# Kernel optimization log

Measured on AMD Instinct MI355X. Metric: run time of the kernel, lower is better.

The kernel has to match this reference:

```python
import jax, jax.numpy as jnp
import numpy as np

N = 100000      # nodes
E = 400000      # edges (before self loops)
D_ATOM = 98
D_BOND = 13
EMB = 128
HEADS = 4
L = 4           # num_layer


def prelu(x, a):
    return jnp.where(x >= 0, x, a * x)


def setup_inputs() -> dict:
    key = jax.random.key(0)
    ks = jax.random.split(key, 12)
    s = 0.05
    inp = {
        "x": jax.random.normal(ks[0], (N, D_ATOM), dtype=jnp.float32),
        "edge_index": jax.random.randint(ks[1], (2, E), 0, N, dtype=jnp.int64),
        "edge_attr": jax.random.uniform(ks[2], (E, D_BOND), dtype=jnp.float32),
        # GNN-level params
        "x_emb_W": jax.random.normal(ks[3], (D_ATOM, EMB), dtype=jnp.float32) * s,
        "prelu_gnn": jnp.float32(0.25),
        # per-layer GATConv params, stacked on leading layer axis
        "wl_W": jax.random.normal(ks[4], (L, EMB, HEADS * EMB), dtype=jnp.float32) * s,
        "wl_b": jnp.zeros((L, HEADS * EMB), dtype=jnp.float32),
        "att": jax.random.normal(ks[5], (L, HEADS, 2 * EMB), dtype=jnp.float32) * s,
        "gat_bias": jnp.zeros((L, EMB), dtype=jnp.float32),
        "ee_W": jax.random.normal(ks[6], (L, D_BOND, HEADS * EMB), dtype=jnp.float32) * s,
        "ee_b": jnp.zeros((L, HEADS * EMB), dtype=jnp.float32),
        "prelu_gat": jnp.full((L,), 0.25, dtype=jnp.float32),
        # LayerNorm params per layer
        "ln_g": jnp.ones((L, EMB), dtype=jnp.float32),
        "ln_b": jnp.zeros((L, EMB), dtype=jnp.float32),
    }
    return inp


def reference(x, edge_index, edge_attr, x_emb_W, prelu_gnn, wl_W, wl_b, att,
              gat_bias, ee_W, ee_b, prelu_gat, ln_g, ln_b):
    # add self loops: (i, i) for every node; self-loop edge_attr = zeros
    loop = jnp.arange(N, dtype=edge_index.dtype)
    src = jnp.concatenate([edge_index[0], loop])  # [E+N] source (j)
    dst = jnp.concatenate([edge_index[1], loop])  # [E+N] target (i)
    ea = jnp.concatenate(
        [edge_attr, jnp.zeros((N, D_BOND), dtype=edge_attr.dtype)], axis=0)

    # input embedding + shared PReLU
    h = prelu(x @ x_emb_W, prelu_gnn)  # [N, EMB]

    for l in range(L):
        a = prelu_gat[l]
        ee = prelu(ea @ ee_W[l] + ee_b[l], a)       # [E+N, H*EMB]
        xw = prelu(h @ wl_W[l] + wl_b[l], a)        # [N, H*EMB]
        x_i = xw[dst].reshape(-1, HEADS, EMB)       # target feats
        x_j = (xw[src] + ee).reshape(-1, HEADS, EMB)  # source feats + edge emb
        # attention logits: cat([x_i,x_j]) . att
        alpha = (x_i * att[l, :, :EMB]).sum(-1) + (x_j * att[l, :, EMB:]).sum(-1)
        alpha = prelu(alpha, a)                     # [E+N, HEADS]
        # segment softmax grouped by src (edge_index[0]), as in the module
        m = jax.ops.segment_max(alpha, src, num_segments=N)
        alpha = jnp.exp(alpha - m[src])
        ssum = jax.ops.segment_sum(alpha, src, num_segments=N)
        alpha = alpha / (ssum[src] + 1e-16)
        # weighted messages, scatter-add to target nodes
        msg = (x_j * alpha[:, :, None]).reshape(-1, HEADS * EMB)
        aggr = jax.ops.segment_sum(msg, dst, num_segments=N)
        aggr = aggr.reshape(N, HEADS, EMB).mean(axis=1) + gat_bias[l]
        # LayerNorm
        mu = aggr.mean(-1, keepdims=True)
        var = ((aggr - mu) ** 2).mean(-1, keepdims=True)
        hn = (aggr - mu) / jnp.sqrt(var + 1e-5) * ln_g[l] + ln_b[l]
        # dropout is identity (drop_ratio=0); PReLU on all but last layer
        h = hn if l == L - 1 else prelu(hn, prelu_gnn)

    return h  # JK='last'
```

## Files before the change

### kernel.cpp

```cpp
#include <hip/hip_runtime.h>
#include <stdint.h>

#define NN 100000
#define NE 400000
#define NT 500000
#define DA 98
#define DB 13
#define EMB 128
#define HE 512
#define NWAVE 8192
#define IMSK 0x0FFFFFFF

typedef unsigned short ushort_t;
typedef __bf16 bf16x8 __attribute__((ext_vector_type(8)));
typedef float floatx4 __attribute__((ext_vector_type(4)));
typedef __fp16 fp16v2 __attribute__((ext_vector_type(2)));

__device__ __forceinline__ float prelu_f(float x, float a) { return x >= 0.f ? x : a * x; }

__device__ __forceinline__ ushort_t f2bf(float f) {
    unsigned u = __float_as_uint(f);
    unsigned r = (u + 0x7fffu + ((u >> 16) & 1u)) >> 16;
    return (ushort_t)r;
}
__device__ __forceinline__ float bflo(unsigned u) { return __uint_as_float(u << 16); }
__device__ __forceinline__ float bfhi(unsigned u) { return __uint_as_float(u & 0xffff0000u); }

__device__ __forceinline__ float dot2(unsigned a, unsigned b, float c) {
    return __builtin_amdgcn_fdot2(__builtin_bit_cast(fp16v2, a), __builtin_bit_cast(fp16v2, b), c, false);
}

__device__ __forceinline__ unsigned pk2(float lo, float hi) {
    fp16v2 p = __builtin_amdgcn_cvt_pkrtz(lo, hi);
    return __builtin_bit_cast(unsigned, p);
}

__global__ void k_count(const int* __restrict__ ei, int* __restrict__ sc, int* __restrict__ dc) {
    int e = blockIdx.x * 256 + threadIdx.x;
    if (e >= NT) return;
    int s, d;
    if (e < NE) { s = ei[e]; d = ei[NE + e]; } else { s = d = e - NE; }
    atomicAdd(sc + s, 1);
    atomicAdd(dc + d, 1);
}

__global__ void k_scan1(const int* __restrict__ cnt, int* __restrict__ part, int* __restrict__ bsum) {
    __shared__ int tmp[512];
    int t = threadIdx.x, i = blockIdx.x * 512 + t;
    int v = (i < NN) ? cnt[i] : 0;
    tmp[t] = v;
    __syncthreads();
    for (int off = 1; off < 512; off <<= 1) {
        int x = (t >= off) ? tmp[t - off] : 0;
        __syncthreads();
        tmp[t] += x;
        __syncthreads();
    }
    if (i < NN) part[i] = tmp[t] - v;
    if (t == 511) bsum[blockIdx.x] = tmp[t];
}

__global__ void k_scan2(int* __restrict__ bsum, int nb) {
    __shared__ int tmp[256];
    int t = threadIdx.x;
    int v = (t < nb) ? bsum[t] : 0;
    tmp[t] = v;
    __syncthreads();
    for (int off = 1; off < 256; off <<= 1) {
        int x = (t >= off) ? tmp[t - off] : 0;
        __syncthreads();
        tmp[t] += x;
        __syncthreads();
    }
    if (t < nb) bsum[t] = tmp[t] - v;
}

__global__ void k_scan3(const int* __restrict__ part, const int* __restrict__ bsum,
                        int* __restrict__ off, int* __restrict__ cur) {
    int i = blockIdx.x * 256 + threadIdx.x;
    if (i < NN) {
        int v = part[i] + bsum[i >> 9];
        off[i] = v;
        cur[i] = v;
    }
    if (i == 0) off[NN] = NT;
}

__global__ void k_fill(const int* __restrict__ ei, int* __restrict__ scur, int* __restrict__ dcur,
                       int* __restrict__ seid, int* __restrict__ deid) {
    int e = blockIdx.x * 256 + threadIdx.x;
    if (e >= NT) return;
    int s, d;
    if (e < NE) { s = ei[e]; d = ei[NE + e]; } else { s = d = e - NE; }
    seid[atomicAdd(scur + s, 1)] = e;
    deid[atomicAdd(dcur + d, 1)] = e;
}

__global__ void k_invperm(const int* __restrict__ seid, int* __restrict__ s2p) {
    int i = blockIdx.x * 256 + threadIdx.x;
    if (i < NT) s2p[seid[i]] = i;
}

__global__ void k_wrange(const int* __restrict__ offs, int* __restrict__ nstart) {
    int w = blockIdx.x * 256 + threadIdx.x;
    if (w > NWAVE) return;
    long long target = (long long)w * NT / NWAVE;
    int lo = 0, hi = NN;
    while (lo < hi) {
        int mid = (lo + hi) >> 1;
        if ((long long)offs[mid] < target) lo = mid + 1; else hi = mid;
    }
    nstart[w] = lo;
}

__global__ void k_dprep(const int* __restrict__ deid, const int* __restrict__ ei,
                        const float* __restrict__ ea, const int* __restrict__ s2p,
                        int* __restrict__ src_d, int* __restrict__ d2s,
                        unsigned* __restrict__ ea_d) {
    int i = blockIdx.x * 256 + threadIdx.x;
    if (i >= NT + 4) return;
    unsigned p[8] = {0, 0, 0, 0, 0, 0, 0, 0};
    int s = 0, pos = 0;
    if (i < NT) {
        int eid = deid[i];
        if (eid < NE) {
            s = ei[eid];
            float v[DB];
            #pragma unroll
            for (int k = 0; k < DB; ++k) v[k] = ea[(size_t)eid * DB + k];
            #pragma unroll
            for (int kp = 0; kp < 6; ++kp) p[kp] = pk2(v[2 * kp], v[2 * kp + 1]);
            p[6] = pk2(v[12], 0.f);
        } else {
            s = (eid - NE) | (1 << 30);
        }
        pos = s2p[eid];
    }
    uint4* o = (uint4*)&ea_d[(size_t)i * 8];
    o[0] = make_uint4(p[0], p[1], p[2], p[3]);
    o[1] = make_uint4(p[4], p[5], p[6], p[7]);
    src_d[i] = s;
    d2s[i] = pos;
}

__global__ void k_sprep(const int* __restrict__ seid, const int* __restrict__ ei,
                        const float* __restrict__ ea,
                        int* __restrict__ dst_s, unsigned* __restrict__ ea_s) {
    int i = blockIdx.x * 256 + threadIdx.x;
    if (i >= NT + 4) return;
    unsigned p[8] = {0, 0, 0, 0, 0, 0, 0, 0};
    int d = 0;
    if (i < NT) {
        int eid = seid[i];
        if (eid < NE) {
            d = ei[NE + eid];
            float v[DB];
            #pragma unroll
            for (int k = 0; k < DB; ++k) v[k] = ea[(size_t)eid * DB + k];
            #pragma unroll
            for (int kp = 0; kp < 6; ++kp) p[kp] = pk2(v[2 * kp], v[2 * kp + 1]);
            p[6] = pk2(v[12], 0.f);
        } else {
            d = (eid - NE) | (1 << 30);
        }
    }
    uint4* o = (uint4*)&ea_s[(size_t)i * 8];
    o[0] = make_uint4(p[0], p[1], p[2], p[3]);
    o[1] = make_uint4(p[4], p[5], p[6], p[7]);
    dst_s[i] = d;
}

__global__ void k_prep_x(const float* __restrict__ x, ushort_t* __restrict__ xb) {
    int idx = blockIdx.x * 256 + threadIdx.x;
    if (idx >= NN * 128) return;
    int col = idx & 127, n = idx >> 7;
    float v = (col < DA) ? x[(size_t)n * DA + col] : 0.f;
    xb[idx] = f2bf(v);
}

__global__ void k_prep_wx(const float* __restrict__ W, ushort_t* __restrict__ Wxt) {
    int idx = blockIdx.x * 256 + threadIdx.x;
    if (idx >= 128 * 128) return;
    int k = idx & 127, n = idx >> 7;
    float v = (k < DA) ? W[(size_t)k * EMB + n] : 0.f;
    Wxt[idx] = f2bf(v);
}

__global__ __launch_bounds__(256) void k_embed_m(const ushort_t* __restrict__ xb, const ushort_t* __restrict__ Wxt,
                                                 const float* __restrict__ pg, ushort_t* __restrict__ hb) {
    __shared__ ushort_t At[64 * 136];
    __shared__ ushort_t Bt[128 * 136];
    int t = threadIdx.x;
    int m0 = blockIdx.x * 64;
    for (int idx = t; idx < 64 * 16; idx += 256) {
        int r = idx >> 4, co = (idx & 15) * 8;
        int gr = m0 + r; if (gr >= NN) gr = 0;
        *(uint4*)&At[r * 136 + co] = *(const uint4*)&xb[(size_t)gr * 128 + co];
    }
    for (int idx = t; idx < 128 * 16; idx += 256) {
        int n = idx >> 4, ko = (idx & 15) * 8;
        *(uint4*)&Bt[n * 136 + ko] = *(const uint4*)&Wxt[n * 128 + ko];
    }
    float p = pg[0];
    __syncthreads();

    int wv = t >> 6, lane = t & 63;
    int ml = lane & 15, kq = lane >> 4;
    int n0w = wv * 32;
    floatx4 acc[4][2];
    #pragma unroll
    for (int mt = 0; mt < 4; ++mt)
        #pragma unroll
        for (int nt = 0; nt < 2; ++nt)
            acc[mt][nt] = (floatx4){0.f, 0.f, 0.f, 0.f};

    #pragma unroll
    for (int k0 = 0; k0 < 128; k0 += 32) {
        bf16x8 af[4], bfv[2];
        #pragma unroll
        for (int mt = 0; mt < 4; ++mt) {
            uint4 u = *(const uint4*)&At[(mt * 16 + ml) * 136 + k0 + kq * 8];
            af[mt] = __builtin_bit_cast(bf16x8, u);
        }
        #pragma unroll
        for (int nt = 0; nt < 2; ++nt) {
            uint4 u = *(const uint4*)&Bt[(n0w + nt * 16 + ml) * 136 + k0 + kq * 8];
            bfv[nt] = __builtin_bit_cast(bf16x8, u);
        }
        #pragma unroll
        for (int mt = 0; mt < 4; ++mt)
            #pragma unroll
            for (int nt = 0; nt < 2; ++nt)
                acc[mt][nt] = __builtin_amdgcn_mfma_f32_16x16x32_bf16(af[mt], bfv[nt], acc[mt][nt], 0, 0, 0);
    }
    #pragma unroll
    for (int nt = 0; nt < 2; ++nt) {
        int col = n0w + nt * 16 + ml;
        #pragma unroll
        for (int mt = 0; mt < 4; ++mt) {
            int row = m0 + mt * 16 + kq * 4;
            #pragma unroll
            for (int q = 0; q < 4; ++q) {
                int r = row + q;
                if (r < NN) hb[(size_t)r * EMB + col] = f2bf(prelu_f(acc[mt][nt][q], p));
            }
        }
    }
}

__global__ void k_prep(const float* __restrict__ wlW, ushort_t* __restrict__ Wtg) {
    int idx = blockIdx.x * 256 + threadIdx.x;
    if (idx >= 4 * 512 * 128) return;
    int k = idx & 127;
    int n = (idx >> 7) & 511;
    int l = idx >> 16;
    Wtg[idx] = f2bf(wlW[(size_t)l * 65536 + k * 512 + n]);
}

__global__ void k_prep_eep(const float* __restrict__ eeW, unsigned* __restrict__ eeWp) {
    int idx = blockIdx.x * 256 + threadIdx.x;
    if (idx >= 4 * 7 * 512) return;
    int l = idx / 3584;
    int rem = idx - l * 3584;
    int kp = rem >> 9;
    int ch = rem & 511;
    float lo = eeW[((size_t)l * DB + 2 * kp) * HE + ch];
    float hi = (2 * kp + 1 < DB) ? eeW[((size_t)l * DB + 2 * kp + 1) * HE + ch] : 0.f;
    eeWp[idx] = pk2(lo, hi);
}

__global__ __launch_bounds__(256) void k_gemm(const ushort_t* __restrict__ hb, const ushort_t* __restrict__ Wtg,
                                              const float* __restrict__ bl, const float* __restrict__ pa,
                                              const float* __restrict__ attl,
                                              ushort_t* __restrict__ xw,
                                              float* __restrict__ ddst, float* __restrict__ dsrc) {
    __shared__ ushort_t At[64 * 136];
    __shared__ ushort_t Bt[128 * 136];
    int t = threadIdx.x;
    int m0 = blockIdx.x * 64;
    int h = blockIdx.y;
    int n0 = h * 128;
    for (int idx = t; idx < 64 * 16; idx += 256) {
        int r = idx >> 4, co = (idx & 15) * 8;
        int gr = m0 + r; if (gr >= NN) gr = 0;
        *(uint4*)&At[r * 136 + co] = *(const uint4*)&hb[(size_t)gr * EMB + co];
    }
    for (int idx = t; idx < 128 * 16; idx += 256) {
        int n = idx >> 4, ko = (idx & 15) * 8;
        *(uint4*)&Bt[n * 136 + ko] = *(const uint4*)&Wtg[(size_t)(n0 + n) * 128 + ko];
    }
    float a = pa[0];
    __syncthreads();

    int wv = t >> 6, lane = t & 63;
    int ml = lane & 15, kq = lane >> 4;
    int n0w = wv * 32;
    floatx4 acc[4][2];
    #pragma unroll
    for (int mt = 0; mt < 4; ++mt)
        #pragma unroll
        for (int nt = 0; nt < 2; ++nt)
            acc[mt][nt] = (floatx4){0.f, 0.f, 0.f, 0.f};

    #pragma unroll
    for (int k0 = 0; k0 < 128; k0 += 32) {
        bf16x8 af[4], bfv[2];
        #pragma unroll
        for (int mt = 0; mt < 4; ++mt) {
            uint4 u = *(const uint4*)&At[(mt * 16 + ml) * 136 + k0 + kq * 8];
            af[mt] = __builtin_bit_cast(bf16x8, u);
        }
        #pragma unroll
        for (int nt = 0; nt < 2; ++nt) {
            uint4 u = *(const uint4*)&Bt[(n0w + nt * 16 + ml) * 136 + k0 + kq * 8];
            bfv[nt] = __builtin_bit_cast(bf16x8, u);
        }
        #pragma unroll
        for (int mt = 0; mt < 4; ++mt)
            #pragma unroll
            for (int nt = 0; nt < 2; ++nt)
                acc[mt][nt] = __builtin_amdgcn_mfma_f32_16x16x32_bf16(af[mt], bfv[nt], acc[mt][nt], 0, 0, 0);
    }
    __syncthreads();
    float* sdd = (float*)At;
    float* sds = (float*)At + 256;

    float pd[4][4], ps[4][4];
    #pragma unroll
    for (int mt = 0; mt < 4; ++mt)
        #pragma unroll
        for (int q = 0; q < 4; ++q) { pd[mt][q] = 0.f; ps[mt][q] = 0.f; }

    #pragma unroll
    for (int nt = 0; nt < 2; ++nt) {
        int ch = n0w + nt * 16 + ml;
        int col = n0 + ch;
        float bv = bl[col];
        float a1v = attl[h * 256 + ch];
        float a2v = attl[h * 256 + 128 + ch];
        #pragma unroll
        for (int mt = 0; mt < 4; ++mt) {
            int row = m0 + mt * 16 + kq * 4;
            #pragma unroll
            for (int q = 0; q < 4; ++q) {
                int r = row + q;
                float v = prelu_f(acc[mt][nt][q] + bv, a);
                if (r < NN) xw[(size_t)r * HE + col] = f2bf(v);
                pd[mt][q] += v * a1v;
                ps[mt][q] += v * a2v;
            }
        }
    }
    #pragma unroll
    for (int mt = 0; mt < 4; ++mt)
        #pragma unroll
        for (int q = 0; q < 4; ++q) {
            float d = pd[mt][q], s = ps[mt][q];
            #pragma unroll
            for (int m = 1; m < 16; m <<= 1) {
                d += __shfl_xor(d, m, 64);
                s += __shfl_xor(s, m, 64);
            }
            if (ml == 0) {
                int lr = mt * 16 + kq * 4 + q;
                sdd[wv * 64 + lr] = d;
                sds[wv * 64 + lr] = s;
            }
        }
    __syncthreads();
    if (t < 64) {
        int r = m0 + t;
        if (r < NN) {
            float d = sdd[t] + sdd[64 + t] + sdd[128 + t] + sdd[192 + t];
            float s = sds[t] + sds[64 + t] + sds[128 + t] + sds[192 + t];
            ddst[r * 4 + h] = d;
            dsrc[r * 4 + h] = s;
        }
    }
}

__global__ __launch_bounds__(256) void k_edgesm(const int* __restrict__ nstart_s,
                                                const int* __restrict__ soff,
                                                const unsigned* __restrict__ ea_s,
                                                const int* __restrict__ dst_s,
                                                const unsigned* __restrict__ eeWp, const float* __restrict__ ebl,
                                                const float* __restrict__ attl, const float* __restrict__ pa,
                                                const float* __restrict__ ddst, const float* __restrict__ dsrc,
                                                float* __restrict__ alpha_s) {
    int t = threadIdx.x;
    float a = pa[0];
    int lane = t & 63;
    int w = blockIdx.x * 4 + (t >> 6);
    int hd = lane >> 4;
    int cm = (lane & 15) * 8;
    int c0 = lane * 8;
    uint4 wpa[7], wpb[7];
    #pragma unroll
    for (int kp = 0; kp < 7; ++kp) {
        wpa[kp] = *(const uint4*)&eeWp[kp * HE + c0];
        wpb[kp] = *(const uint4*)&eeWp[kp * HE + c0 + 4];
    }
    float a2[8], eb[8];
    #pragma unroll
    for (int q = 0; q < 8; ++q) {
        a2[q] = attl[hd * 256 + 128 + cm + q];
        eb[q] = ebl[c0 + q];
    }
    float pselfR = 0.f;
    #pragma unroll
    for (int q = 0; q < 8; ++q) pselfR += prelu_f(eb[q], a) * a2[q];
    #pragma unroll
    for (int m = 1; m < 16; m <<= 1) pselfR += __shfl_xor(pselfR, m, 64);

    int head = lane & 3;
    int slot = lane >> 2;

    int n0 = nstart_s[w], n1 = nstart_s[w + 1];
    if (n0 >= n1) return;
    int e0 = soff[n0], e1 = soff[n1];

    uint4 eaAa = *(const uint4*)&ea_s[(size_t)e0 * 8];
    uint4 eaAb = *(const uint4*)&ea_s[(size_t)e0 * 8 + 4];
    int rA = dst_s[e0], rB = dst_s[e0 + 1];
    int dA = rA & IMSK, fA = rA >> 30;
    int dB = rB & IMSK, fB = rB >> 30;
    float diA = ddst[dA * 4 + hd];

    int n = n0;
    int b = e0;
    int bEnd = soff[n0 + 1];
    bool small = (bEnd - b) <= 16;
    float sj = dsrc[n * 4 + hd];
    float mx = -1e30f;
    float myLg = -1e30f;

    for (int i = e0; i < e1; ++i) {
        uint4 eaNa = *(const uint4*)&ea_s[(size_t)(i + 1) * 8];
        uint4 eaNb = *(const uint4*)&ea_s[(size_t)(i + 1) * 8 + 4];
        int rC = dst_s[i + 2];
        int dC = rC & IMSK, fC = rC >> 30;
        float diB = ddst[dB * 4 + hd];
        float p;
        if (__builtin_amdgcn_readfirstlane(fA)) {
            p = pselfR;
        } else {
            unsigned ec[7] = {eaAa.x, eaAa.y, eaAa.z, eaAa.w, eaAb.x, eaAb.y, eaAb.z};
            float v[8];
            #pragma unroll
            for (int q = 0; q < 8; ++q) v[q] = eb[q];
            #pragma unroll
            for (int kp = 0; kp < 7; ++kp) {
                v[0] = dot2(ec[kp], wpa[kp].x, v[0]);
                v[1] = dot2(ec[kp], wpa[kp].y, v[1]);
                v[2] = dot2(ec[kp], wpa[kp].z, v[2]);
                v[3] = dot2(ec[kp], wpa[kp].w, v[3]);
                v[4] = dot2(ec[kp], wpb[kp].x, v[4]);
                v[5] = dot2(ec[kp], wpb[kp].y, v[5]);
                v[6] = dot2(ec[kp], wpb[kp].z, v[6]);
                v[7] = dot2(ec[kp], wpb[kp].w, v[7]);
            }
            p = 0.f;
            #pragma unroll
            for (int q = 0; q < 8; ++q) p += prelu_f(v[q], a) * a2[q];
            #pragma unroll
            for (int m = 1; m < 16; m <<= 1) p += __shfl_xor(p, m, 64);
        }
        float lg = prelu_f(diA + sj + p, a);
        if (small) {
            float lgH = __shfl(lg, head * 16, 64);
            myLg = (slot == (i - b)) ? lgH : myLg;
        } else {
            if ((lane & 15) == 0) {
                alpha_s[(size_t)i * 4 + hd] = lg;
                mx = fmaxf(mx, lg);
            }
        }
        if (i + 1 == bEnd) {
            if (small) {
                float mh = myLg;
                #pragma unroll
                for (int m = 4; m < 64; m <<= 1) mh = fmaxf(mh, __shfl_xor(mh, m, 64));
                float ex = __expf(myLg - mh);
                float s = ex;
                #pragma unroll
                for (int m = 4; m < 64; m <<= 1) s += __shfl_xor(s, m, 64);
                float inv = 1.f / (s + 1e-16f);
                if (slot < bEnd - b)
                    alpha_s[(size_t)(b + slot) * 4 + head] = ex * inv;
            } else {
                float m0v = __shfl(mx, 0, 64), m1v = __shfl(mx, 16, 64),
                      m2v = __shfl(mx, 32, 64), m3v = __shfl(mx, 48, 64);
                float mh = head == 0 ? m0v : head == 1 ? m1v : head == 2 ? m2v : m3v;
                asm volatile("s_waitcnt vmcnt(0)" ::: "memory");
                float s = 0.f;
                for (int idx = b + (lane >> 2); idx < bEnd; idx += 16) {
                    float x = alpha_s[(size_t)idx * 4 + head];
                    float ex = __expf(x - mh);
                    s += ex;
                    alpha_s[(size_t)idx * 4 + head] = ex;
                }
                #pragma unroll
                for (int m = 4; m < 64; m <<= 1) s += __shfl_xor(s, m, 64);
                float inv = 1.f / (s + 1e-16f);
                asm volatile("s_waitcnt vmcnt(0)" ::: "memory");
                for (int idx = b + (lane >> 2); idx < bEnd; idx += 16)
                    alpha_s[(size_t)idx * 4 + head] *= inv;
            }
            ++n;
            if (i + 1 < e1) {
                b = bEnd;
                bEnd = soff[n + 1];
                small = (bEnd - b) <= 16;
                sj = dsrc[n * 4 + hd];
                mx = -1e30f;
                myLg = -1e30f;
            }
        }
        eaAa = eaNa; eaAb = eaNb;
        dA = dB; fA = fB;
        dB = dC; fB = fC;
        diA = diB;
    }
}

__global__ __launch_bounds__(256) void k_aggr(const int* __restrict__ nstart,
                                              const int* __restrict__ doff,
                                              const int* __restrict__ src_d, const int* __restrict__ d2s,
                                              const unsigned* __restrict__ ea_d,
                                              const unsigned* __restrict__ eeWp, const float* __restrict__ ebl,
                                              const float* __restrict__ pa, const ushort_t* __restrict__ xw,
                                              const float* __restrict__ alpha_s,
                                              const float* __restrict__ gbias, const float* __restrict__ lng,
                                              const float* __restrict__ lnb, const float* __restrict__ pgnn,
                                              int last, ushort_t* __restrict__ hb_out, float* __restrict__ fout) {
    int t = threadIdx.x;
    float a = pa[0], pg = pgnn[0];
    int lane = t & 63;
    int w = blockIdx.x * 4 + (t >> 6);
    int hd = lane >> 4;
    int cm = (lane & 15) * 8;
    int c0 = lane * 8;
    uint4 wpa[7], wpb[7];
    #pragma unroll
    for (int kp = 0; kp < 7; ++kp) {
        wpa[kp] = *(const uint4*)&eeWp[kp * HE + c0];
        wpb[kp] = *(const uint4*)&eeWp[kp * HE + c0 + 4];
    }
    float eb[8], ebp[8];
    #pragma unroll
    for (int q = 0; q < 8; ++q) {
        eb[q] = ebl[c0 + q];
        ebp[q] = prelu_f(eb[q], a);
    }

    int n0 = nstart[w], n1 = nstart[w + 1];
    if (n0 >= n1) return;
    int e0 = doff[n0];
    int e1 = doff[n1];

    int rA = src_d[e0], rB = src_d[e0 + 1], rN = src_d[e0 + 2];
    int sA = rA & IMSK, fA = rA >> 30;
    int sB = rB & IMSK, fB = rB >> 30;
    int sN = rN & IMSK, fN = rN >> 30;
    int pA = d2s[e0], pB = d2s[e0 + 1], pN = d2s[e0 + 2];
    uint4 xwA = *(const uint4*)&xw[(size_t)sA * HE + c0];
    float alA = alpha_s[(size_t)pA * 4 + hd];
    uint4 xwB = *(const uint4*)&xw[(size_t)sB * HE + c0];
    float alB = alpha_s[(size_t)pB * 4 + hd];
    uint4 eaCa = *(const uint4*)&ea_d[(size_t)e0 * 8];
    uint4 eaCb = *(const uint4*)&ea_d[(size_t)e0 * 8 + 4];

    int n = n0;
    int b1 = doff[n0 + 1];
    int nn2 = (n0 + 2 <= NN) ? n0 + 2 : NN;
    int b2 = doff[nn2];
    float acc[8] = {0.f, 0.f, 0.f, 0.f, 0.f, 0.f, 0.f, 0.f};

    for (int i = e0; i < e1; ++i) {
        uint4 eaNa = *(const uint4*)&ea_d[(size_t)(i + 1) * 8];
        uint4 eaNb = *(const uint4*)&ea_d[(size_t)(i + 1) * 8 + 4];
        uint4 xwC = *(const uint4*)&xw[(size_t)sN * HE + c0];
        float alC = alpha_s[(size_t)pN * 4 + hd];
        int rN2 = src_d[i + 3];
        int sN2 = rN2 & IMSK, fN2 = rN2 >> 30;
        int pN2 = d2s[i + 3];
        float pw[8];
        if (__builtin_amdgcn_readfirstlane(fA)) {
            #pragma unroll
            for (int q = 0; q < 8; ++q) pw[q] = ebp[q];
        } else {
            unsigned ec[7] = {eaCa.x, eaCa.y, eaCa.z, eaCa.w, eaCb.x, eaCb.y, eaCb.z};
            float wv[8];
            #pragma unroll
            for (int q = 0; q < 8; ++q) wv[q] = eb[q];
            #pragma unroll
            for (int kp = 0; kp < 7; ++kp) {
                wv[0] = dot2(ec[kp], wpa[kp].x, wv[0]);
                wv[1] = dot2(ec[kp], wpa[kp].y, wv[1]);
                wv[2] = dot2(ec[kp], wpa[kp].z, wv[2]);
                wv[3] = dot2(ec[kp], wpa[kp].w, wv[3]);
                wv[4] = dot2(ec[kp], wpb[kp].x, wv[4]);
                wv[5] = dot2(ec[kp], wpb[kp].y, wv[5]);
                wv[6] = dot2(ec[kp], wpb[kp].z, wv[6]);
                wv[7] = dot2(ec[kp], wpb[kp].w, wv[7]);
            }
            #pragma unroll
            for (int q = 0; q < 8; ++q) pw[q] = prelu_f(wv[q], a);
        }
        float xv[8] = {bflo(xwA.x), bfhi(xwA.x), bflo(xwA.y), bfhi(xwA.y),
                       bflo(xwA.z), bfhi(xwA.z), bflo(xwA.w), bfhi(xwA.w)};
        #pragma unroll
        for (int q = 0; q < 8; ++q) acc[q] += (xv[q] + pw[q]) * alA;
        if (i + 1 == b1) {
            float gbv[8], gv[8], bbv[8];
            *(float4*)&gbv[0] = *(const float4*)&gbias[cm];
            *(float4*)&gbv[4] = *(const float4*)&gbias[cm + 4];
            *(float4*)&gv[0]  = *(const float4*)&lng[cm];
            *(float4*)&gv[4]  = *(const float4*)&lng[cm + 4];
            *(float4*)&bbv[0] = *(const float4*)&lnb[cm];
            *(float4*)&bbv[4] = *(const float4*)&lnb[cm + 4];
            float hm[8];
            #pragma unroll
            for (int q = 0; q < 8; ++q) {
                float v = acc[q];
                v += __shfl_xor(v, 16, 64);
                v += __shfl_xor(v, 32, 64);
                hm[q] = 0.25f * v + gbv[q];
            }
            float s8 = 0.f, q8 = 0.f;
            #pragma unroll
            for (int q = 0; q < 8; ++q) { s8 += hm[q]; q8 += hm[q] * hm[q]; }
            #pragma unroll
            for (int m = 1; m < 16; m <<= 1) {
                s8 += __shfl_xor(s8, m, 64);
                q8 += __shfl_xor(q8, m, 64);
            }
            float mu = s8 * (1.f / 128.f);
            float var = q8 * (1.f / 128.f) - mu * mu;
            float rstd = rsqrtf(var + 1e-5f);
            if (lane < 16) {
                float o[8];
                #pragma unroll
                for (int q = 0; q < 8; ++q) {
                    float v = (hm[q] - mu) * rstd * gv[q] + bbv[q];
                    o[q] = last ? v : prelu_f(v, pg);
                }
                if (last) {
                    float4* op = (float4*)&fout[(size_t)n * EMB + lane * 8];
                    op[0] = make_float4(o[0], o[1], o[2], o[3]);
                    op[1] = make_float4(o[4], o[5], o[6], o[7]);
                } else {
                    uint4 ob;
                    ob.x = (unsigned)f2bf(o[0]) | ((unsigned)f2bf(o[1]) << 16);
                    ob.y = (unsigned)f2bf(o[2]) | ((unsigned)f2bf(o[3]) << 16);
                    ob.z = (unsigned)f2bf(o[4]) | ((unsigned)f2bf(o[5]) << 16);
                    ob.w = (unsigned)f2bf(o[6]) | ((unsigned)f2bf(o[7]) << 16);
                    *(uint4*)&hb_out[(size_t)n * EMB + lane * 8] = ob;
                }
            }
            #pragma unroll
            for (int q = 0; q < 8; ++q) acc[q] = 0.f;
            ++n;
            b1 = b2;
            int nx = (n + 2 <= NN) ? n + 2 : NN;
            b2 = doff[nx];
        }
        xwA = xwB; alA = alB;
        xwB = xwC; alB = alC;
        sN = sN2; pN = pN2;
        fA = fB; fB = fN; fN = fN2;
        eaCa = eaNa; eaCb = eaNb;
    }
}

extern "C" void kernel_launch(void* const* d_in, const int* in_sizes, int n_in,
                              void* d_out, int out_size, void* d_ws, size_t ws_size,
                              hipStream_t stream) {
    const float* x     = (const float*)d_in[0];
    const int*   ei    = (const int*)d_in[1];
    const float* ea    = (const float*)d_in[2];
    const float* xembW = (const float*)d_in[3];
    const float* pgnn  = (const float*)d_in[4];
    const float* wlW   = (const float*)d_in[5];
    const float* wlb   = (const float*)d_in[6];
    const float* att   = (const float*)d_in[7];
    const float* gbias = (const float*)d_in[8];
    const float* eeW   = (const float*)d_in[9];
    const float* eeb   = (const float*)d_in[10];
    const float* pgat  = (const float*)d_in[11];
    const float* lng   = (const float*)d_in[12];
    const float* lnb   = (const float*)d_in[13];

    char* w = (char*)d_ws;
    size_t off = 0;
    auto alloc = [&](size_t nbytes) -> char* {
        char* p = w + off;
        off += (nbytes + 255) & ~(size_t)255;
        return p;
    };
    ushort_t* hb    = (ushort_t*)alloc((size_t)NN * EMB * 2);
    ushort_t* xw    = (ushort_t*)alloc((size_t)NN * HE * 2);
    ushort_t* Wtg   = (ushort_t*)alloc((size_t)4 * 512 * 128 * 2);
    ushort_t* Wxt   = (ushort_t*)alloc((size_t)128 * 128 * 2);
    unsigned* eeWp  = (unsigned*)alloc((size_t)4 * 7 * 512 * 4);
    float*    ddst  = (float*)alloc((size_t)NN * 4 * 4);
    float*    dsrc  = (float*)alloc((size_t)NN * 4 * 4);
    float*    alpha = (float*)alloc((size_t)NT * 4 * 4);
    unsigned* ea_d  = (unsigned*)alloc((size_t)(NT + 4) * 8 * 4);
    unsigned* ea_s  = (unsigned*)alloc((size_t)(NT + 4) * 8 * 4);
    int* scnt     = (int*)alloc((size_t)NN * 4);
    int* dcnt     = (int*)alloc((size_t)NN * 4);
    int* soff     = (int*)alloc((size_t)(NN + 1) * 4);
    int* doff     = (int*)alloc((size_t)(NN + 1) * 4);
    int* scur     = (int*)alloc((size_t)NN * 4);
    int* dcur     = (int*)alloc((size_t)NN * 4);
    int* seid     = (int*)alloc((size_t)NT * 4);
    int* deid     = (int*)alloc((size_t)NT * 4);
    int* s2p      = (int*)alloc((size_t)NT * 4);
    int* src_d    = (int*)alloc((size_t)(NT + 4) * 4);
    int* d2s      = (int*)alloc((size_t)(NT + 4) * 4);
    int* dst_s    = (int*)alloc((size_t)(NT + 4) * 4);
    int* nstart   = (int*)alloc((size_t)(NWAVE + 1) * 4);
    int* nstart_s = (int*)alloc((size_t)(NWAVE + 1) * 4);
    int* part     = (int*)alloc((size_t)NN * 4);
    int* bsum     = (int*)alloc(256 * 4);

    ushort_t* xb = xw;

    hipMemsetAsync(scnt, 0, (size_t)NN * 4, stream);
    hipMemsetAsync(dcnt, 0, (size_t)NN * 4, stream);
    k_count<<<(NT + 255) / 256, 256, 0, stream>>>(ei, scnt, dcnt);
    k_scan1<<<196, 512, 0, stream>>>(scnt, part, bsum);
    k_scan2<<<1, 256, 0, stream>>>(bsum, 196);
    k_scan3<<<391, 256, 0, stream>>>(part, bsum, soff, scur);
    k_scan1<<<196, 512, 0, stream>>>(dcnt, part, bsum);
    k_scan2<<<1, 256, 0, stream>>>(bsum, 196);
    k_scan3<<<391, 256, 0, stream>>>(part, bsum, doff, dcur);
    k_fill<<<(NT + 255) / 256, 256, 0, stream>>>(ei, scur, dcur, seid, deid);
    k_invperm<<<(NT + 255) / 256, 256, 0, stream>>>(seid, s2p);
    k_wrange<<<(NWAVE + 1 + 255) / 256, 256, 0, stream>>>(doff, nstart);
    k_wrange<<<(NWAVE + 1 + 255) / 256, 256, 0, stream>>>(soff, nstart_s);
    k_dprep<<<(NT + 4 + 255) / 256, 256, 0, stream>>>(deid, ei, ea, s2p, src_d, d2s, ea_d);
    k_sprep<<<(NT + 4 + 255) / 256, 256, 0, stream>>>(seid, ei, ea, dst_s, ea_s);
    k_prep_x<<<(NN * 128 + 255) / 256, 256, 0, stream>>>(x, xb);
    k_prep_wx<<<(128 * 128 + 255) / 256, 256, 0, stream>>>(xembW, Wxt);
    k_embed_m<<<(NN + 63) / 64, 256, 0, stream>>>(xb, Wxt, pgnn, hb);
    k_prep<<<(4 * 512 * 128 + 255) / 256, 256, 0, stream>>>(wlW, Wtg);
    k_prep_eep<<<(4 * 7 * 512 + 255) / 256, 256, 0, stream>>>(eeW, eeWp);

    for (int l = 0; l < 4; ++l) {
        const float* bl  = wlb + (size_t)l * HE;
        const float* al  = att + (size_t)l * 1024;
        const unsigned* eWl = eeWp + (size_t)l * 7 * HE;
        const float* ebl = eeb + (size_t)l * HE;
        const float* pa  = pgat + l;
        const ushort_t* Wt = Wtg + (size_t)l * 512 * 128;
        k_gemm<<<dim3((NN + 63) / 64, 4), 256, 0, stream>>>(hb, Wt, bl, pa, al, xw, ddst, dsrc);
        k_edgesm<<<2048, 256, 0, stream>>>(nstart_s, soff, ea_s, dst_s, eWl, ebl, al, pa,
                                           ddst, dsrc, alpha);
        k_aggr<<<2048, 256, 0, stream>>>(nstart, doff, src_d, d2s, ea_d, eWl, ebl, pa, xw, alpha,
                                         gbias + (size_t)l * EMB, lng + (size_t)l * EMB,
                                         lnb + (size_t)l * EMB, pgnn, (l == 3) ? 1 : 0,
                                         hb, (float*)d_out);
    }
}
```

Baseline: 1.804 ms.

## Merge preprocessing kernels, pack edge index pairs, hoist LayerNorm param loads

```diff
diff --git a/kernel.cpp b/kernel.cpp
--- a/kernel.cpp
+++ b/kernel.cpp
@@ -87,36 +87,39 @@
 }
 
 __global__ void k_fill(const int* __restrict__ ei, int* __restrict__ scur, int* __restrict__ dcur,
-                       int* __restrict__ seid, int* __restrict__ deid) {
+                       int* __restrict__ seid, int* __restrict__ deid, int* __restrict__ s2p) {
     int e = blockIdx.x * 256 + threadIdx.x;
     if (e >= NT) return;
     int s, d;
     if (e < NE) { s = ei[e]; d = ei[NE + e]; } else { s = d = e - NE; }
-    seid[atomicAdd(scur + s, 1)] = e;
+    int p = atomicAdd(scur + s, 1);
+    seid[p] = e;
+    s2p[e] = p;
     deid[atomicAdd(dcur + d, 1)] = e;
 }
 
-__global__ void k_invperm(const int* __restrict__ seid, int* __restrict__ s2p) {
-    int i = blockIdx.x * 256 + threadIdx.x;
-    if (i < NT) s2p[seid[i]] = i;
-}
-
-__global__ void k_wrange(const int* __restrict__ offs, int* __restrict__ nstart) {
+__global__ void k_wrange2(const int* __restrict__ doff, const int* __restrict__ soff,
+                          int* __restrict__ nstart, int* __restrict__ nstart_s) {
     int w = blockIdx.x * 256 + threadIdx.x;
     if (w > NWAVE) return;
     long long target = (long long)w * NT / NWAVE;
     int lo = 0, hi = NN;
     while (lo < hi) {
         int mid = (lo + hi) >> 1;
-        if ((long long)offs[mid] < target) lo = mid + 1; else hi = mid;
+        if ((long long)doff[mid] < target) lo = mid + 1; else hi = mid;
     }
     nstart[w] = lo;
+    lo = 0; hi = NN;
+    while (lo < hi) {
+        int mid = (lo + hi) >> 1;
+        if ((long long)soff[mid] < target) lo = mid + 1; else hi = mid;
+    }
+    nstart_s[w] = lo;
 }
 
 __global__ void k_dprep(const int* __restrict__ deid, const int* __restrict__ ei,
                         const float* __restrict__ ea, const int* __restrict__ s2p,
-                        int* __restrict__ src_d, int* __restrict__ d2s,
-                        unsigned* __restrict__ ea_d) {
+                        int2* __restrict__ sd_d, unsigned* __restrict__ ea_d) {
     int i = blockIdx.x * 256 + threadIdx.x;
     if (i >= NT + 4) return;
     unsigned p[8] = {0, 0, 0, 0, 0, 0, 0, 0};
@@ -139,8 +142,7 @@
     uint4* o = (uint4*)&ea_d[(size_t)i * 8];
     o[0] = make_uint4(p[0], p[1], p[2], p[3]);
     o[1] = make_uint4(p[4], p[5], p[6], p[7]);
-    src_d[i] = s;
-    d2s[i] = pos;
+    sd_d[i] = make_int2(s, pos);
 }
 
 __global__ void k_sprep(const int* __restrict__ seid, const int* __restrict__ ei,
@@ -170,21 +172,44 @@
     dst_s[i] = d;
 }
 
-__global__ void k_prep_x(const float* __restrict__ x, ushort_t* __restrict__ xb) {
+__global__ void k_prep_all(const float* __restrict__ x, const float* __restrict__ xembW,
+                           const float* __restrict__ wlW, const float* __restrict__ eeW,
+                           ushort_t* __restrict__ xb, ushort_t* __restrict__ Wxt,
+                           ushort_t* __restrict__ Wtg, unsigned* __restrict__ eeWp) {
     int idx = blockIdx.x * 256 + threadIdx.x;
-    if (idx >= NN * 128) return;
-    int col = idx & 127, n = idx >> 7;
-    float v = (col < DA) ? x[(size_t)n * DA + col] : 0.f;
-    xb[idx] = f2bf(v);
-}
-
-__global__ void k_prep_wx(const float* __restrict__ W, ushort_t* __restrict__ Wxt) {
-    int idx = blockIdx.x * 256 + threadIdx.x;
-    if (idx >= 128 * 128) return;
-    int k = idx & 127, n = idx >> 7;
-    float v = (k < DA) ? W[(size_t)k * EMB + n] : 0.f;
-    Wxt[idx] = f2bf(v);
-}
+    if (idx < NN * 128) {
+        int col = idx & 127, n = idx >> 7;
+        float v = (col < DA) ? x[(size_t)n * DA + col] : 0.f;
+        xb[idx] = f2bf(v);
+        return;
+    }
+    idx -= NN * 128;
+    if (idx < 128 * 128) {
+        int k = idx & 127, n = idx >> 7;
+        float v = (k < DA) ? xembW[(size_t)k * EMB + n] : 0.f;
+        Wxt[idx] = f2bf(v);
+        return;
+    }
+    idx -= 128 * 128;
+    if (idx < 4 * 512 * 128) {
+        int k = idx & 127;
+        int n = (idx >> 7) & 511;
+        int l = idx >> 16;
+        Wtg[idx] = f2bf(wlW[(size_t)l * 65536 + k * 512 + n]);
+        return;
+    }
+    idx -= 4 * 512 * 128;
+    if (idx < 4 * 7 * 512) {
+        int l = idx / 3584;
+        int rem = idx - l * 3584;
+        int kp = rem >> 9;
+        int ch = rem & 511;
+        float lo = eeW[((size_t)l * DB + 2 * kp) * HE + ch];
+        float hi = (2 * kp + 1 < DB) ? eeW[((size_t)l * DB + 2 * kp + 1) * HE + ch] : 0.f;
+        eeWp[idx] = pk2(lo, hi);
+    }
+}
+#define PREP_TOTAL (NN * 128 + 128 * 128 + 4 * 512 * 128 + 4 * 7 * 512)
 
 __global__ __launch_bounds__(256) void k_embed_m(const ushort_t* __restrict__ xb, const ushort_t* __restrict__ Wxt,
                                                  const float* __restrict__ pg, ushort_t* __restrict__ hb) {
@@ -246,27 +271,6 @@
             }
         }
     }
-}
-
-__global__ void k_prep(const float* __restrict__ wlW, ushort_t* __restrict__ Wtg) {
-    int idx = blockIdx.x * 256 + threadIdx.x;
-    if (idx >= 4 * 512 * 128) return;
-    int k = idx & 127;
-    int n = (idx >> 7) & 511;
-    int l = idx >> 16;
-    Wtg[idx] = f2bf(wlW[(size_t)l * 65536 + k * 512 + n]);
-}
-
-__global__ void k_prep_eep(const float* __restrict__ eeW, unsigned* __restrict__ eeWp) {
-    int idx = blockIdx.x * 256 + threadIdx.x;
-    if (idx >= 4 * 7 * 512) return;
-    int l = idx / 3584;
-    int rem = idx - l * 3584;
-    int kp = rem >> 9;
-    int ch = rem & 511;
-    float lo = eeW[((size_t)l * DB + 2 * kp) * HE + ch];
-    float hi = (2 * kp + 1 < DB) ? eeW[((size_t)l * DB + 2 * kp + 1) * HE + ch] : 0.f;
-    eeWp[idx] = pk2(lo, hi);
 }
 
 __global__ __launch_bounds__(256) void k_gemm(const ushort_t* __restrict__ hb, const ushort_t* __restrict__ Wtg,
@@ -525,7 +529,7 @@
 
 __global__ __launch_bounds__(256) void k_aggr(const int* __restrict__ nstart,
                                               const int* __restrict__ doff,
-                                              const int* __restrict__ src_d, const int* __restrict__ d2s,
+                                              const int2* __restrict__ sd_d,
                                               const unsigned* __restrict__ ea_d,
                                               const unsigned* __restrict__ eeWp, const float* __restrict__ ebl,
                                               const float* __restrict__ pa, const ushort_t* __restrict__ xw,
@@ -552,17 +556,23 @@
         eb[q] = ebl[c0 + q];
         ebp[q] = prelu_f(eb[q], a);
     }
+    float gbv[8], gv[8], bbv[8];
+    *(float4*)&gbv[0] = *(const float4*)&gbias[cm];
+    *(float4*)&gbv[4] = *(const float4*)&gbias[cm + 4];
+    *(float4*)&gv[0]  = *(const float4*)&lng[cm];
+    *(float4*)&gv[4]  = *(const float4*)&lng[cm + 4];
+    *(float4*)&bbv[0] = *(const float4*)&lnb[cm];
+    *(float4*)&bbv[4] = *(const float4*)&lnb[cm + 4];
 
     int n0 = nstart[w], n1 = nstart[w + 1];
     if (n0 >= n1) return;
     int e0 = doff[n0];
     int e1 = doff[n1];
 
-    int rA = src_d[e0], rB = src_d[e0 + 1], rN = src_d[e0 + 2];
-    int sA = rA & IMSK, fA = rA >> 30;
-    int sB = rB & IMSK, fB = rB >> 30;
-    int sN = rN & IMSK, fN = rN >> 30;
-    int pA = d2s[e0], pB = d2s[e0 + 1], pN = d2s[e0 + 2];
+    int2 rA = sd_d[e0], rB = sd_d[e0 + 1], rN = sd_d[e0 + 2];
+    int sA = rA.x & IMSK, fA = rA.x >> 30, pA = rA.y;
+    int sB = rB.x & IMSK, fB = rB.x >> 30, pB = rB.y;
+    int sN = rN.x & IMSK, fN = rN.x >> 30, pN = rN.y;
     uint4 xwA = *(const uint4*)&xw[(size_t)sA * HE + c0];
     float alA = alpha_s[(size_t)pA * 4 + hd];
     uint4 xwB = *(const uint4*)&xw[(size_t)sB * HE + c0];
@@ -581,9 +591,8 @@
         uint4 eaNb = *(const uint4*)&ea_d[(size_t)(i + 1) * 8 + 4];
         uint4 xwC = *(const uint4*)&xw[(size_t)sN * HE + c0];
         float alC = alpha_s[(size_t)pN * 4 + hd];
-        int rN2 = src_d[i + 3];
-        int sN2 = rN2 & IMSK, fN2 = rN2 >> 30;
-        int pN2 = d2s[i + 3];
+        int2 rN2 = sd_d[i + 3];
+        int sN2 = rN2.x & IMSK, fN2 = rN2.x >> 30, pN2 = rN2.y;
         float pw[8];
         if (__builtin_amdgcn_readfirstlane(fA)) {
             #pragma unroll
@@ -612,13 +621,6 @@
         #pragma unroll
         for (int q = 0; q < 8; ++q) acc[q] += (xv[q] + pw[q]) * alA;
         if (i + 1 == b1) {
-            float gbv[8], gv[8], bbv[8];
-            *(float4*)&gbv[0] = *(const float4*)&gbias[cm];
-            *(float4*)&gbv[4] = *(const float4*)&gbias[cm + 4];
-            *(float4*)&gv[0]  = *(const float4*)&lng[cm];
-            *(float4*)&gv[4]  = *(const float4*)&lng[cm + 4];
-            *(float4*)&bbv[0] = *(const float4*)&lnb[cm];
-            *(float4*)&bbv[4] = *(const float4*)&lnb[cm + 4];
             float hm[8];
             #pragma unroll
             for (int q = 0; q < 8; ++q) {
@@ -708,8 +710,10 @@
     float*    alpha = (float*)alloc((size_t)NT * 4 * 4);
     unsigned* ea_d  = (unsigned*)alloc((size_t)(NT + 4) * 8 * 4);
     unsigned* ea_s  = (unsigned*)alloc((size_t)(NT + 4) * 8 * 4);
-    int* scnt     = (int*)alloc((size_t)NN * 4);
-    int* dcnt     = (int*)alloc((size_t)NN * 4);
+    int2* sd_d    = (int2*)alloc((size_t)(NT + 4) * 8);
+    int* cnt2     = (int*)alloc((size_t)2 * NN * 4);
+    int* scnt     = cnt2;
+    int* dcnt     = cnt2 + NN;
     int* soff     = (int*)alloc((size_t)(NN + 1) * 4);
     int* doff     = (int*)alloc((size_t)(NN + 1) * 4);
     int* scur     = (int*)alloc((size_t)NN * 4);
@@ -717,8 +721,6 @@
     int* seid     = (int*)alloc((size_t)NT * 4);
     int* deid     = (int*)alloc((size_t)NT * 4);
     int* s2p      = (int*)alloc((size_t)NT * 4);
-    int* src_d    = (int*)alloc((size_t)(NT + 4) * 4);
-    int* d2s      = (int*)alloc((size_t)(NT + 4) * 4);
     int* dst_s    = (int*)alloc((size_t)(NT + 4) * 4);
     int* nstart   = (int*)alloc((size_t)(NWAVE + 1) * 4);
     int* nstart_s = (int*)alloc((size_t)(NWAVE + 1) * 4);
@@ -727,8 +729,7 @@
 
     ushort_t* xb = xw;
 
-    hipMemsetAsync(scnt, 0, (size_t)NN * 4, stream);
-    hipMemsetAsync(dcnt, 0, (size_t)NN * 4, stream);
+    hipMemsetAsync(cnt2, 0, (size_t)2 * NN * 4, stream);
     k_count<<<(NT + 255) / 256, 256, 0, stream>>>(ei, scnt, dcnt);
     k_scan1<<<196, 512, 0, stream>>>(scnt, part, bsum);
     k_scan2<<<1, 256, 0, stream>>>(bsum, 196);
@@ -736,17 +737,12 @@
     k_scan1<<<196, 512, 0, stream>>>(dcnt, part, bsum);
     k_scan2<<<1, 256, 0, stream>>>(bsum, 196);
     k_scan3<<<391, 256, 0, stream>>>(part, bsum, doff, dcur);
-    k_fill<<<(NT + 255) / 256, 256, 0, stream>>>(ei, scur, dcur, seid, deid);
-    k_invperm<<<(NT + 255) / 256, 256, 0, stream>>>(seid, s2p);
-    k_wrange<<<(NWAVE + 1 + 255) / 256, 256, 0, stream>>>(doff, nstart);
-    k_wrange<<<(NWAVE + 1 + 255) / 256, 256, 0, stream>>>(soff, nstart_s);
-    k_dprep<<<(NT + 4 + 255) / 256, 256, 0, stream>>>(deid, ei, ea, s2p, src_d, d2s, ea_d);
+    k_fill<<<(NT + 255) / 256, 256, 0, stream>>>(ei, scur, dcur, seid, deid, s2p);
+    k_wrange2<<<(NWAVE + 1 + 255) / 256, 256, 0, stream>>>(doff, soff, nstart, nstart_s);
+    k_dprep<<<(NT + 4 + 255) / 256, 256, 0, stream>>>(deid, ei, ea, s2p, sd_d, ea_d);
     k_sprep<<<(NT + 4 + 255) / 256, 256, 0, stream>>>(seid, ei, ea, dst_s, ea_s);
-    k_prep_x<<<(NN * 128 + 255) / 256, 256, 0, stream>>>(x, xb);
-    k_prep_wx<<<(128 * 128 + 255) / 256, 256, 0, stream>>>(xembW, Wxt);
+    k_prep_all<<<(PREP_TOTAL + 255) / 256, 256, 0, stream>>>(x, xembW, wlW, eeW, xb, Wxt, Wtg, eeWp);
     k_embed_m<<<(NN + 63) / 64, 256, 0, stream>>>(xb, Wxt, pgnn, hb);
-    k_prep<<<(4 * 512 * 128 + 255) / 256, 256, 0, stream>>>(wlW, Wtg);
-    k_prep_eep<<<(4 * 7 * 512 + 255) / 256, 256, 0, stream>>>(eeW, eeWp);
 
     for (int l = 0; l < 4; ++l) {
         const float* bl  = wlb + (size_t)l * HE;
@@ -758,7 +754,7 @@
         k_gemm<<<dim3((NN + 63) / 64, 4), 256, 0, stream>>>(hb, Wt, bl, pa, al, xw, ddst, dsrc);
         k_edgesm<<<2048, 256, 0, stream>>>(nstart_s, soff, ea_s, dst_s, eWl, ebl, al, pa,
                                            ddst, dsrc, alpha);
-        k_aggr<<<2048, 256, 0, stream>>>(nstart, doff, src_d, d2s, ea_d, eWl, ebl, pa, xw, alpha,
+        k_aggr<<<2048, 256, 0, stream>>>(nstart, doff, sd_d, ea_d, eWl, ebl, pa, xw, alpha,
                                          gbias + (size_t)l * EMB, lng + (size_t)l * EMB,
                                          lnb + (size_t)l * EMB, pgnn, (l == 3) ? 1 : 0,
                                          hb, (float*)d_out);
```

Measured after the change: 1.747 ms. 3.1% less time.
